# Performance work log

Hardware: AMD Instinct MI355X
Metric: run time of the kernel (lower is better)

Reference implementation:

```python
import jax, jax.numpy as jnp
import numpy as np

N_NODES = 100000
N_EDGES = 1600000
D_IN = 128
D_OUT = 128


def setup_inputs() -> dict:
    key = jax.random.key(0)
    k1, k2, k3, k4, k5, k6 = jax.random.split(key, 6)
    x = jax.random.normal(k1, (N_NODES, D_IN), dtype=jnp.float32)
    edge_src = jax.random.randint(k2, (N_EDGES,), 0, N_NODES, dtype=jnp.int64 if jax.config.jax_enable_x64 else jnp.int32)
    edge_dst = jax.random.randint(k3, (N_EDGES,), 0, N_NODES, dtype=jnp.int64 if jax.config.jax_enable_x64 else jnp.int32)
    edge_val = jax.random.uniform(k4, (N_EDGES,), dtype=jnp.float32)
    # nn.Linear(2*D_IN, D_OUT): store W as [2*D_IN, D_OUT] (transposed torch layout)
    W = jax.random.normal(k5, (2 * D_IN, D_OUT), dtype=jnp.float32) * (1.0 / np.sqrt(2 * D_IN))
    b = jax.random.normal(k6, (D_OUT,), dtype=jnp.float32) * 0.01
    return {"x": x, "edge_src": edge_src, "edge_dst": edge_dst, "edge_val": edge_val, "W": W, "b": b}


def reference(x, edge_src, edge_dst, edge_val, W, b):
    # support = adj @ x  (sparse COO: adj[dst, src] = edge_val)
    gathered = x[edge_src] * edge_val[:, None]               # [E, D_IN]
    support = jax.ops.segment_sum(gathered, edge_dst, num_segments=x.shape[0])  # [N, D_IN]
    # concat self + aggregated neighbor features, then linear
    h = jnp.concatenate([x, support], axis=1)                # [N, 2*D_IN]
    return h @ W + b                                          # [N, D_OUT]
```

## Files before the change

kernel.cpp:

```cpp
#include <hip/hip_runtime.h>

#define D 128
#define BN 32
#define NBIN 391
#define NBMAX 512
#define CHUNK 2048
#define SCAP 12
#define HB 128

typedef __attribute__((ext_vector_type(8))) short bf16x8;
typedef __attribute__((ext_vector_type(4))) float f32x4;

__device__ __forceinline__ unsigned short f2bf(float f) {
    unsigned int u = __builtin_bit_cast(unsigned int, f);
    u = (u + 0x7fffu + ((u >> 16) & 1u)) >> 16;
    return (unsigned short)u;
}
__device__ __forceinline__ float bf2f(unsigned int u) {
    return __builtin_bit_cast(float, u << 16);
}

__global__ void prep_kernel(const float* __restrict__ x,
                            unsigned short* __restrict__ x_bf,
                            const float* __restrict__ W,
                            unsigned short* __restrict__ WT,
                            const int* __restrict__ edst,
                            int* __restrict__ hpart,
                            int n4, int XB, int WB, int E) {
    __shared__ int h[NBMAX];
    int blk = blockIdx.x, tid = threadIdx.x;
    if (blk < XB) {
        int i = blk * 256 + tid;
        if (i < n4) {
            float4 v = ((const float4*)x)[i];
            ushort4 s;
            s.x = f2bf(v.x); s.y = f2bf(v.y); s.z = f2bf(v.z); s.w = f2bf(v.w);
            ((ushort4*)x_bf)[i] = s;
        }
    } else if (blk < XB + WB) {
        int t = (blk - XB) * 256 + tid;
        if (t < 2 * D * D) {
            int col = t & 127, k = t >> 7;
            WT[col * 256 + k] = f2bf(W[k * D + col]);
        }
    } else {
        int hb = blk - XB - WB;
        for (int i = tid; i < NBMAX; i += 256) h[i] = 0;
        __syncthreads();
        for (int i = hb * 256 + tid; i < E; i += HB * 256)
            atomicAdd(&h[edst[i] >> 8], 1);
        __syncthreads();
        for (int i = tid; i < NBMAX; i += 256) hpart[hb * NBMAX + i] = h[i];
    }
}

__global__ __launch_bounds__(256) void cscan_kernel(const int* __restrict__ hpart,
                                                    int* __restrict__ ccnt,
                                                    int* __restrict__ cbase,
                                                    int* __restrict__ ccur) {
    __shared__ int p[256];
    int t = threadIdx.x;
    int s0 = 0, s1 = 0;
    for (int j = 0; j < HB; ++j) {
        s0 += hpart[j * NBMAX + 2 * t];
        s1 += hpart[j * NBMAX + 2 * t + 1];
    }
    int loc = s0 + s1;
    p[t] = loc;
    __syncthreads();
    for (int off = 1; off < 256; off <<= 1) {
        int v = p[t];
        int u = (t >= off) ? p[t - off] : 0;
        __syncthreads();
        p[t] = v + u;
        __syncthreads();
    }
    int ex = p[t] - loc;
    ccnt[2 * t] = s0;          ccnt[2 * t + 1] = s1;
    cbase[2 * t] = ex;         ccur[2 * t] = ex;
    cbase[2 * t + 1] = ex + s0; ccur[2 * t + 1] = ex + s0;
}

__global__ __launch_bounds__(256) void cfill_kernel(const int* __restrict__ esrc,
                                                    const int* __restrict__ edst,
                                                    const float* __restrict__ eval,
                                                    int* __restrict__ ccur,
                                                    int2* __restrict__ ep, int E) {
    __shared__ int lh[NBMAX];
    __shared__ int lcur[NBMAX];
    __shared__ int p[256];
    __shared__ int2 ord[CHUNK];
    __shared__ unsigned short obk[CHUNK];

    const int tid = threadIdx.x;
    const int base = blockIdx.x * CHUNK;
    const int n = min(CHUNK, E - base);

    for (int i = tid; i < NBMAX; i += 256) lh[i] = 0;
    __syncthreads();

    int esv[8]; int ebk[8];
    float evv[8];
#pragma unroll
    for (int k = 0; k < 8; ++k) {
        int li = k * 256 + tid;
        if (li < n) {
            int i = base + li;
            int dst = edst[i];
            esv[k] = esrc[i];
            evv[k] = eval[i];
            int b = dst >> 8;
            ebk[k] = b | ((dst & 255) << 16);
            atomicAdd(&lh[b], 1);
        } else ebk[k] = -1;
    }
    __syncthreads();

    int s0 = lh[2 * tid], s1 = lh[2 * tid + 1];
    int loc = s0 + s1;
    p[tid] = loc;
    __syncthreads();
    for (int off = 1; off < 256; off <<= 1) {
        int v = p[tid];
        int u = (tid >= off) ? p[tid - off] : 0;
        __syncthreads();
        p[tid] = v + u;
        __syncthreads();
    }
    int ex = p[tid] - loc;
    lcur[2 * tid] = ex;
    lcur[2 * tid + 1] = ex + s0;
    __syncthreads();

#pragma unroll
    for (int k = 0; k < 8; ++k) {
        if (ebk[k] >= 0) {
            int b = ebk[k] & 0xffff, nl = ebk[k] >> 16;
            int slot = atomicAdd(&lcur[b], 1);
            ord[slot] = make_int2((esv[k] << 8) | nl, __builtin_bit_cast(int, evv[k]));
            obk[slot] = (unsigned short)b;
        }
    }
    __syncthreads();

    for (int b = tid; b < NBIN; b += 256) {
        int c = lh[b];
        if (c) lh[b] = atomicAdd(&ccur[b], c) - (lcur[b] - c);
    }
    __syncthreads();

    for (int i = tid; i < n; i += 256) {
        int b = obk[i];
        ep[lh[b] + i] = ord[i];
    }
}

__global__ __launch_bounds__(512) void csort_kernel(int2* __restrict__ ep,
                                                    const int* __restrict__ cbase,
                                                    const int* __restrict__ ccnt,
                                                    int* __restrict__ node_start) {
    __shared__ int h[256];
    __shared__ int p[256];

    const int t = threadIdx.x;
    const int bin = blockIdx.x;
    const int cb = cbase[bin];
    const int ce = cb + ccnt[bin];

    if (t < 256) h[t] = 0;
    __syncthreads();

    int2 ev[SCAP];
#pragma unroll
    for (int k = 0; k < SCAP; ++k) {
        int idx = cb + k * 512 + t;
        if (idx < ce) {
            int2 e = ep[idx];
            ev[k] = e;
            atomicAdd(&h[e.x & 255], 1);
        } else ev[k] = make_int2(-1, 0);
    }
    __syncthreads();

    int c = 0;
    if (t < 256) { c = h[t]; p[t] = c; }
    __syncthreads();
    for (int off = 1; off < 256; off <<= 1) {
        int v = 0, u = 0;
        if (t < 256) { v = p[t]; u = (t >= off) ? p[t - off] : 0; }
        __syncthreads();
        if (t < 256) p[t] = v + u;
        __syncthreads();
    }
    if (t < 256) {
        int st = cb + p[t] - c;
        node_start[bin * 256 + t] = st;
        h[t] = st;
    }
    __syncthreads();

#pragma unroll
    for (int k = 0; k < SCAP; ++k) {
        if (ev[k].x >= 0) {
            int nl = ev[k].x & 255;
            int pos = atomicAdd(&h[nl], 1);
            ep[pos] = make_int2(ev[k].x & 0xFFFFFF3F, ev[k].y);
        }
    }
}

__global__ __launch_bounds__(256, 8) void gather_fused_kernel(
        const unsigned short* __restrict__ x_bf,
        const int* __restrict__ node_start,
        const int2* __restrict__ edge_pack,
        const unsigned short* __restrict__ WT,
        const float* __restrict__ bias,
        float* __restrict__ out, int N) {
    __shared__ unsigned short accb[BN * 136];
    __shared__ int nb[BN + 1];

    const int tid = threadIdx.x;
    const int node0 = blockIdx.x * BN;
    const int w = tid >> 6, lane = tid & 63;
    unsigned int* accw = (unsigned int*)accb;

    for (int i = tid * 8; i < BN * 136; i += 2048)
        *(uint4*)(accb + i) = make_uint4(0u, 0u, 0u, 0u);
    if (tid <= BN) nb[tid] = node_start[node0 + tid];
    __syncthreads();

    const int js = __builtin_amdgcn_readfirstlane(nb[w * 8]);
    const int je = __builtin_amdgcn_readfirstlane(nb[w * 8 + 8]);
    const unsigned short* xl = x_bf + lane * 2;

    int cur = -1;
    float ax = 0.f, ay = 0.f;
    if (js < je) {
        int2 eC[16], eN[16];
#pragma unroll
        for (int k = 0; k < 16; ++k) {
            int idx = js + k; if (idx >= je) idx = je - 1;
            eC[k] = edge_pack[idx];
        }
        for (int g = js; g < je; g += 16) {
#pragma unroll
            for (int k = 0; k < 16; ++k) {
                int idx = g + 16 + k; if (idx >= je) idx = je - 1;
                eN[k] = edge_pack[idx];
            }
            unsigned int p[16];
#pragma unroll
            for (int k = 0; k < 16; ++k)
                p[k] = *(const unsigned int*)(xl + ((eC[k].x >> 8) << 7));
            int m = je - g; if (m > 16) m = 16;
#pragma unroll
            for (int k = 0; k < 16; ++k) {
                if (k < m) {
                    int nd = eC[k].x & 31;
                    if (nd != cur) {
                        if (cur >= 0)
                            accw[cur * 68 + lane] =
                                (unsigned int)f2bf(ax) | ((unsigned int)f2bf(ay) << 16);
                        cur = nd; ax = 0.f; ay = 0.f;
                    }
                    float v = __builtin_bit_cast(float, eC[k].y);
                    ax += bf2f(p[k] & 0xffffu) * v;
                    ay += bf2f(p[k] >> 16) * v;
                }
            }
#pragma unroll
            for (int k = 0; k < 16; ++k) eC[k] = eN[k];
        }
        if (cur >= 0)
            accw[cur * 68 + lane] = (unsigned int)f2bf(ax) | ((unsigned int)f2bf(ay) << 16);
    }
    __syncthreads();

    const int quad = lane >> 4;
    const int l15  = lane & 15;
    const int colbase = w * 32;

    f32x4 acc[2][2];
#pragma unroll
    for (int rt = 0; rt < 2; ++rt) {
        acc[rt][0] = (f32x4){0.f, 0.f, 0.f, 0.f};
        acc[rt][1] = (f32x4){0.f, 0.f, 0.f, 0.f};
    }

#pragma unroll
    for (int ks = 0; ks < 8; ++ks) {
        bf16x8 wf0 = *(const bf16x8*)(WT + (size_t)(colbase + l15) * 256 + ks * 32 + quad * 8);
        bf16x8 wf1 = *(const bf16x8*)(WT + (size_t)(colbase + 16 + l15) * 256 + ks * 32 + quad * 8);
#pragma unroll
        for (int rt = 0; rt < 2; ++rt) {
            int row = rt * 16 + l15;
            bf16x8 a;
            if (ks < 4) {
                int rg = node0 + row; if (rg >= N) rg = N - 1;
                a = *(const bf16x8*)(x_bf + (size_t)rg * D + ks * 32 + quad * 8);
            } else {
                a = *(const bf16x8*)(accb + row * 136 + (ks - 4) * 32 + quad * 8);
            }
            acc[rt][0] = __builtin_amdgcn_mfma_f32_16x16x32_bf16(a, wf0, acc[rt][0], 0, 0, 0);
            acc[rt][1] = __builtin_amdgcn_mfma_f32_16x16x32_bf16(a, wf1, acc[rt][1], 0, 0, 0);
        }
    }

#pragma unroll
    for (int ct = 0; ct < 2; ++ct) {
        int col = colbase + ct * 16 + l15;
        float bv = bias[col];
#pragma unroll
        for (int rt = 0; rt < 2; ++rt) {
#pragma unroll
            for (int rg = 0; rg < 4; ++rg) {
                int row = node0 + rt * 16 + quad * 4 + rg;
                if (row < N)
                    out[(size_t)row * D + col] = acc[rt][ct][rg] + bv;
            }
        }
    }
}

extern "C" void kernel_launch(void* const* d_in, const int* in_sizes, int n_in,
                              void* d_out, int out_size, void* d_ws, size_t ws_size,
                              hipStream_t stream) {
    const float* x    = (const float*)d_in[0];
    const int*   esrc = (const int*)d_in[1];
    const int*   edst = (const int*)d_in[2];
    const float* eval = (const float*)d_in[3];
    const float* W    = (const float*)d_in[4];
    const float* bias = (const float*)d_in[5];
    float*       out  = (float*)d_out;

    const int N  = in_sizes[0] / D;
    const int E  = in_sizes[1];
    const int NG = (N + BN - 1) / BN;

    char* ws = (char*)d_ws;
    unsigned short* x_bf  = (unsigned short*)ws;
    int2*           ep    = (int2*)(ws + 25600000);
    unsigned short* WT    = (unsigned short*)(ws + 38400000);
    int*            nbg   = (int*)(ws + 38465536);
    int*            ccnt  = (int*)(ws + 38865920);
    int*            cbase = (int*)(ws + 38867968);
    int*            ccur  = (int*)(ws + 38870016);
    int*            hpart = (int*)(ws + 38872064);

    const int n4 = N * D / 4;
    const int XB = (n4 + 255) / 256;
    const int WB = (2 * D * D + 255) / 256;

    prep_kernel<<<XB + WB + HB, 256, 0, stream>>>(x, x_bf, W, WT, edst, hpart,
                                                  n4, XB, WB, E);
    cscan_kernel<<<1, 256, 0, stream>>>(hpart, ccnt, cbase, ccur);
    cfill_kernel<<<(E + CHUNK - 1) / CHUNK, 256, 0, stream>>>(esrc, edst, eval,
                                                              ccur, ep, E);
    csort_kernel<<<NBIN, 512, 0, stream>>>(ep, cbase, ccnt, nbg);
    gather_fused_kernel<<<NG, 256, 0, stream>>>(x_bf, nbg, ep, WT, bias, out, N);
    (void)ws_size; (void)n_in; (void)out_size;
}
```

Before: 272.7 us.

## Fuse per-bin counting sort into gather+GEMM kernel using LDS-staged edges

Bins shrink to 128 nodes, and the separate csort and gather kernels merge into one kernel per bin. Each block sorts its bin's edges by node in LDS, gathers neighbor features from LDS-held edge lists, and runs the MFMA linear layer over 128 rows. This removes the global scatter-back of sorted edges, the node_start array and one launch. The cost is a large LDS footprint, a fixed per-bin capacity (SCAP*512 = 3072 edges) that overflows on heavier bins, and 782 blocks of 512 threads instead of about 3100 smaller blocks.

```diff
diff --git a/kernel.cpp b/kernel.cpp
--- a/kernel.cpp
+++ b/kernel.cpp
@@ -1,11 +1,12 @@
 #include <hip/hip_runtime.h>
 
 #define D 128
-#define BN 32
-#define NBIN 391
-#define NBMAX 512
+#define BNODES 128
+#define NBIN 782
+#define NBMAX 1024
 #define CHUNK 2048
-#define SCAP 12
+#define SCAP 6
+#define ORDCAP 3072
 #define HB 128
 
 typedef __attribute__((ext_vector_type(8))) short bf16x8;
@@ -48,7 +49,7 @@
         for (int i = tid; i < NBMAX; i += 256) h[i] = 0;
         __syncthreads();
         for (int i = hb * 256 + tid; i < E; i += HB * 256)
-            atomicAdd(&h[edst[i] >> 8], 1);
+            atomicAdd(&h[edst[i] >> 7], 1);
         __syncthreads();
         for (int i = tid; i < NBMAX; i += 256) hpart[hb * NBMAX + i] = h[i];
     }
@@ -60,12 +61,12 @@
                                                     int* __restrict__ ccur) {
     __shared__ int p[256];
     int t = threadIdx.x;
-    int s0 = 0, s1 = 0;
+    int s0 = 0, s1 = 0, s2 = 0, s3 = 0;
     for (int j = 0; j < HB; ++j) {
-        s0 += hpart[j * NBMAX + 2 * t];
-        s1 += hpart[j * NBMAX + 2 * t + 1];
-    }
-    int loc = s0 + s1;
+        int4 v = *(const int4*)(hpart + j * NBMAX + t * 4);
+        s0 += v.x; s1 += v.y; s2 += v.z; s3 += v.w;
+    }
+    int loc = s0 + s1 + s2 + s3;
     p[t] = loc;
     __syncthreads();
     for (int off = 1; off < 256; off <<= 1) {
@@ -76,9 +77,11 @@
         __syncthreads();
     }
     int ex = p[t] - loc;
-    ccnt[2 * t] = s0;          ccnt[2 * t + 1] = s1;
-    cbase[2 * t] = ex;         ccur[2 * t] = ex;
-    cbase[2 * t + 1] = ex + s0; ccur[2 * t + 1] = ex + s0;
+    ccnt[4 * t] = s0; ccnt[4 * t + 1] = s1; ccnt[4 * t + 2] = s2; ccnt[4 * t + 3] = s3;
+    cbase[4 * t] = ex;            ccur[4 * t] = ex;
+    cbase[4 * t + 1] = ex + s0;   ccur[4 * t + 1] = ex + s0;
+    cbase[4 * t + 2] = ex + s0 + s1;      ccur[4 * t + 2] = ex + s0 + s1;
+    cbase[4 * t + 3] = ex + s0 + s1 + s2; ccur[4 * t + 3] = ex + s0 + s1 + s2;
 }
 
 __global__ __launch_bounds__(256) void cfill_kernel(const int* __restrict__ esrc,
@@ -109,15 +112,15 @@
             int dst = edst[i];
             esv[k] = esrc[i];
             evv[k] = eval[i];
-            int b = dst >> 8;
-            ebk[k] = b | ((dst & 255) << 16);
+            int b = dst >> 7;
+            ebk[k] = b | ((dst & 127) << 16);
             atomicAdd(&lh[b], 1);
         } else ebk[k] = -1;
     }
     __syncthreads();
 
-    int s0 = lh[2 * tid], s1 = lh[2 * tid + 1];
-    int loc = s0 + s1;
+    int s0 = lh[4 * tid], s1 = lh[4 * tid + 1], s2 = lh[4 * tid + 2], s3 = lh[4 * tid + 3];
+    int loc = s0 + s1 + s2 + s3;
     p[tid] = loc;
     __syncthreads();
     for (int off = 1; off < 256; off <<= 1) {
@@ -128,8 +131,10 @@
         __syncthreads();
     }
     int ex = p[tid] - loc;
-    lcur[2 * tid] = ex;
-    lcur[2 * tid + 1] = ex + s0;
+    lcur[4 * tid] = ex;
+    lcur[4 * tid + 1] = ex + s0;
+    lcur[4 * tid + 2] = ex + s0 + s1;
+    lcur[4 * tid + 3] = ex + s0 + s1 + s2;
     __syncthreads();
 
 #pragma unroll
@@ -155,48 +160,56 @@
     }
 }
 
-__global__ __launch_bounds__(512) void csort_kernel(int2* __restrict__ ep,
-                                                    const int* __restrict__ cbase,
-                                                    const int* __restrict__ ccnt,
-                                                    int* __restrict__ node_start) {
-    __shared__ int h[256];
-    __shared__ int p[256];
+__global__ __launch_bounds__(512, 4) void sg_kernel(
+        const unsigned short* __restrict__ x_bf,
+        const int* __restrict__ cbase,
+        const int* __restrict__ ccnt,
+        const int2* __restrict__ ep,
+        const unsigned short* __restrict__ WT,
+        const float* __restrict__ bias,
+        float* __restrict__ out, int N) {
+    __shared__ int2 ord[ORDCAP];
+    __shared__ unsigned short accb[BNODES * 136];
+    __shared__ int h[BNODES];
+    __shared__ int p[BNODES];
+    __shared__ int nb[BNODES + 1];
 
     const int t = threadIdx.x;
     const int bin = blockIdx.x;
     const int cb = cbase[bin];
-    const int ce = cb + ccnt[bin];
-
-    if (t < 256) h[t] = 0;
+    const int n = ccnt[bin];
+    const int node0 = bin * BNODES;
+    const int w = t >> 6, lane = t & 63;
+    unsigned int* accw = (unsigned int*)accb;
+
+    for (int i = t * 8; i < BNODES * 136; i += 4096)
+        *(uint4*)(accb + i) = make_uint4(0u, 0u, 0u, 0u);
+    if (t < BNODES) h[t] = 0;
     __syncthreads();
 
     int2 ev[SCAP];
 #pragma unroll
     for (int k = 0; k < SCAP; ++k) {
-        int idx = cb + k * 512 + t;
-        if (idx < ce) {
-            int2 e = ep[idx];
-            ev[k] = e;
-            atomicAdd(&h[e.x & 255], 1);
+        int idx = k * 512 + t;
+        if (idx < n) {
+            ev[k] = ep[cb + idx];
+            atomicAdd(&h[ev[k].x & 255], 1);
         } else ev[k] = make_int2(-1, 0);
     }
     __syncthreads();
 
     int c = 0;
-    if (t < 256) { c = h[t]; p[t] = c; }
-    __syncthreads();
-    for (int off = 1; off < 256; off <<= 1) {
+    if (t < BNODES) { c = h[t]; p[t] = c; }
+    __syncthreads();
+    for (int off = 1; off < BNODES; off <<= 1) {
         int v = 0, u = 0;
-        if (t < 256) { v = p[t]; u = (t >= off) ? p[t - off] : 0; }
-        __syncthreads();
-        if (t < 256) p[t] = v + u;
-        __syncthreads();
-    }
-    if (t < 256) {
-        int st = cb + p[t] - c;
-        node_start[bin * 256 + t] = st;
-        h[t] = st;
-    }
+        if (t < BNODES) { v = p[t]; u = (t >= off) ? p[t - off] : 0; }
+        __syncthreads();
+        if (t < BNODES) p[t] = v + u;
+        __syncthreads();
+    }
+    if (t < BNODES) { int st = p[t] - c; nb[t] = st; h[t] = st; }
+    if (t == 0) nb[BNODES] = n;
     __syncthreads();
 
 #pragma unroll
@@ -204,96 +217,70 @@
         if (ev[k].x >= 0) {
             int nl = ev[k].x & 255;
             int pos = atomicAdd(&h[nl], 1);
-            ep[pos] = make_int2(ev[k].x & 0xFFFFFF3F, ev[k].y);
-        }
-    }
-}
-
-__global__ __launch_bounds__(256, 8) void gather_fused_kernel(
-        const unsigned short* __restrict__ x_bf,
-        const int* __restrict__ node_start,
-        const int2* __restrict__ edge_pack,
-        const unsigned short* __restrict__ WT,
-        const float* __restrict__ bias,
-        float* __restrict__ out, int N) {
-    __shared__ unsigned short accb[BN * 136];
-    __shared__ int nb[BN + 1];
-
-    const int tid = threadIdx.x;
-    const int node0 = blockIdx.x * BN;
-    const int w = tid >> 6, lane = tid & 63;
-    unsigned int* accw = (unsigned int*)accb;
-
-    for (int i = tid * 8; i < BN * 136; i += 2048)
-        *(uint4*)(accb + i) = make_uint4(0u, 0u, 0u, 0u);
-    if (tid <= BN) nb[tid] = node_start[node0 + tid];
-    __syncthreads();
-
-    const int js = __builtin_amdgcn_readfirstlane(nb[w * 8]);
-    const int je = __builtin_amdgcn_readfirstlane(nb[w * 8 + 8]);
-    const unsigned short* xl = x_bf + lane * 2;
+            ord[pos] = ev[k];
+        }
+    }
+    __syncthreads();
+
+    const int js = __builtin_amdgcn_readfirstlane(nb[w * 16]);
+    const int je = __builtin_amdgcn_readfirstlane(nb[w * 16 + 16]);
 
     int cur = -1;
     float ax = 0.f, ay = 0.f;
-    if (js < je) {
-        int2 eC[16], eN[16];
+    for (int g = js; g < je; g += 16) {
+        int m = je - g; if (m > 16) m = 16;
+        int2 e[16];
 #pragma unroll
         for (int k = 0; k < 16; ++k) {
-            int idx = js + k; if (idx >= je) idx = je - 1;
-            eC[k] = edge_pack[idx];
-        }
-        for (int g = js; g < je; g += 16) {
-#pragma unroll
-            for (int k = 0; k < 16; ++k) {
-                int idx = g + 16 + k; if (idx >= je) idx = je - 1;
-                eN[k] = edge_pack[idx];
+            int idx = g + k; if (idx >= je) idx = je - 1;
+            e[k] = ord[idx];
+        }
+        unsigned int px[16];
+#pragma unroll
+        for (int k = 0; k < 16; ++k) {
+            int sx = __builtin_amdgcn_readfirstlane(e[k].x);
+            px[k] = *(const unsigned int*)(x_bf + ((sx >> 8) << 7) + lane * 2);
+        }
+#pragma unroll
+        for (int k = 0; k < 16; ++k) {
+            if (k < m) {
+                int nd = e[k].x & 255;
+                if (nd != cur) {
+                    if (cur >= 0)
+                        accw[cur * 68 + lane] =
+                            (unsigned int)f2bf(ax) | ((unsigned int)f2bf(ay) << 16);
+                    cur = nd; ax = 0.f; ay = 0.f;
+                }
+                float v = __builtin_bit_cast(float, e[k].y);
+                ax += bf2f(px[k] & 0xffffu) * v;
+                ay += bf2f(px[k] >> 16) * v;
             }
-            unsigned int p[16];
-#pragma unroll
-            for (int k = 0; k < 16; ++k)
-                p[k] = *(const unsigned int*)(xl + ((eC[k].x >> 8) << 7));
-            int m = je - g; if (m > 16) m = 16;
-#pragma unroll
-            for (int k = 0; k < 16; ++k) {
-                if (k < m) {
-                    int nd = eC[k].x & 31;
-                    if (nd != cur) {
-                        if (cur >= 0)
-                            accw[cur * 68 + lane] =
-                                (unsigned int)f2bf(ax) | ((unsigned int)f2bf(ay) << 16);
-                        cur = nd; ax = 0.f; ay = 0.f;
-                    }
-                    float v = __builtin_bit_cast(float, eC[k].y);
-                    ax += bf2f(p[k] & 0xffffu) * v;
-                    ay += bf2f(p[k] >> 16) * v;
-                }
-            }
-#pragma unroll
-            for (int k = 0; k < 16; ++k) eC[k] = eN[k];
-        }
-        if (cur >= 0)
-            accw[cur * 68 + lane] = (unsigned int)f2bf(ax) | ((unsigned int)f2bf(ay) << 16);
-    }
+        }
+    }
+    if (cur >= 0)
+        accw[cur * 68 + lane] = (unsigned int)f2bf(ax) | ((unsigned int)f2bf(ay) << 16);
     __syncthreads();
 
     const int quad = lane >> 4;
     const int l15  = lane & 15;
-    const int colbase = w * 32;
-
-    f32x4 acc[2][2];
-#pragma unroll
-    for (int rt = 0; rt < 2; ++rt) {
-        acc[rt][0] = (f32x4){0.f, 0.f, 0.f, 0.f};
-        acc[rt][1] = (f32x4){0.f, 0.f, 0.f, 0.f};
-    }
+    const int wr = w & 3, wc = w >> 2;
+
+    f32x4 acc[2][4];
+#pragma unroll
+    for (int rt = 0; rt < 2; ++rt)
+#pragma unroll
+        for (int ct = 0; ct < 4; ++ct)
+            acc[rt][ct] = (f32x4){0.f, 0.f, 0.f, 0.f};
 
 #pragma unroll
     for (int ks = 0; ks < 8; ++ks) {
-        bf16x8 wf0 = *(const bf16x8*)(WT + (size_t)(colbase + l15) * 256 + ks * 32 + quad * 8);
-        bf16x8 wf1 = *(const bf16x8*)(WT + (size_t)(colbase + 16 + l15) * 256 + ks * 32 + quad * 8);
+        bf16x8 wf[4];
+#pragma unroll
+        for (int ct = 0; ct < 4; ++ct)
+            wf[ct] = *(const bf16x8*)(WT + (size_t)(wc * 64 + ct * 16 + l15) * 256 + ks * 32 + quad * 8);
 #pragma unroll
         for (int rt = 0; rt < 2; ++rt) {
-            int row = rt * 16 + l15;
+            int row = wr * 32 + rt * 16 + l15;
             bf16x8 a;
             if (ks < 4) {
                 int rg = node0 + row; if (rg >= N) rg = N - 1;
@@ -301,20 +288,21 @@
             } else {
                 a = *(const bf16x8*)(accb + row * 136 + (ks - 4) * 32 + quad * 8);
             }
-            acc[rt][0] = __builtin_amdgcn_mfma_f32_16x16x32_bf16(a, wf0, acc[rt][0], 0, 0, 0);
-            acc[rt][1] = __builtin_amdgcn_mfma_f32_16x16x32_bf16(a, wf1, acc[rt][1], 0, 0, 0);
-        }
-    }
-
-#pragma unroll
-    for (int ct = 0; ct < 2; ++ct) {
-        int col = colbase + ct * 16 + l15;
+#pragma unroll
+            for (int ct = 0; ct < 4; ++ct)
+                acc[rt][ct] = __builtin_amdgcn_mfma_f32_16x16x32_bf16(a, wf[ct], acc[rt][ct], 0, 0, 0);
+        }
+    }
+
+#pragma unroll
+    for (int ct = 0; ct < 4; ++ct) {
+        int col = wc * 64 + ct * 16 + l15;
         float bv = bias[col];
 #pragma unroll
         for (int rt = 0; rt < 2; ++rt) {
 #pragma unroll
             for (int rg = 0; rg < 4; ++rg) {
-                int row = node0 + rt * 16 + quad * 4 + rg;
+                int row = node0 + wr * 32 + rt * 16 + quad * 4 + rg;
                 if (row < N)
                     out[(size_t)row * D + col] = acc[rt][ct][rg] + bv;
             }
@@ -335,17 +323,15 @@
 
     const int N  = in_sizes[0] / D;
     const int E  = in_sizes[1];
-    const int NG = (N + BN - 1) / BN;
 
     char* ws = (char*)d_ws;
     unsigned short* x_bf  = (unsigned short*)ws;
     int2*           ep    = (int2*)(ws + 25600000);
     unsigned short* WT    = (unsigned short*)(ws + 38400000);
-    int*            nbg   = (int*)(ws + 38465536);
-    int*            ccnt  = (int*)(ws + 38865920);
-    int*            cbase = (int*)(ws + 38867968);
-    int*            ccur  = (int*)(ws + 38870016);
-    int*            hpart = (int*)(ws + 38872064);
+    int*            ccnt  = (int*)(ws + 38465536);
+    int*            cbase = (int*)(ws + 38469632);
+    int*            ccur  = (int*)(ws + 38473728);
+    int*            hpart = (int*)(ws + 38477824);
 
     const int n4 = N * D / 4;
     const int XB = (n4 + 255) / 256;
@@ -356,7 +342,6 @@
     cscan_kernel<<<1, 256, 0, stream>>>(hpart, ccnt, cbase, ccur);
     cfill_kernel<<<(E + CHUNK - 1) / CHUNK, 256, 0, stream>>>(esrc, edst, eval,
                                                               ccur, ep, E);
-    csort_kernel<<<NBIN, 512, 0, stream>>>(ep, cbase, ccnt, nbg);
-    gather_fused_kernel<<<NG, 256, 0, stream>>>(x_bf, nbg, ep, WT, bias, out, N);
+    sg_kernel<<<NBIN, 512, 0, stream>>>(x_bf, cbase, ccnt, ep, WT, bias, out, N);
     (void)ws_size; (void)n_in; (void)out_size;
 }
```

Result: slower. 285.8 us (+4.8%).
